# Performance work log

Measured on AMD Instinct MI355X. Metric: run time of the kernel, lower is better.

## Reference

```python
import jax, jax.numpy as jnp
import numpy as np

# Dimensions (match init_kwargs / input_specs)
B, L, HID, NH, HD, PROJ, NL = 4, 1024, 512, 8, 64, 2048, 2
LN_EPS = 1e-5


def _layer_norm(x, g, b):
    m = x.mean(-1, keepdims=True)
    v = ((x - m) ** 2).mean(-1, keepdims=True)
    return (x - m) / jnp.sqrt(v + LN_EPS) * g + b


def setup_inputs() -> dict:
    key = jax.random.key(0)
    ks = jax.random.split(key, 8)
    layer_x = jax.random.normal(ks[0], (B, L, HID), jnp.float32)
    # causal attention mask (True = masked), as built by mask_reshape (triu(1))
    causal = jnp.triu(jnp.ones((L, L), bool), 1)
    full_mask = jnp.broadcast_to(causal[None], (B, L, L))
    mask_multiplier = jnp.ones((B, L, 1), jnp.float32)
    s = 0.02
    qkv_w = (jax.random.normal(ks[1], (NL, HID, 3 * NH * HD), jnp.float32) * s)
    qkv_b = jnp.zeros((NL, 3 * NH * HD), jnp.float32)
    o_w = jax.random.normal(ks[2], (NL, NH * HD, HID), jnp.float32) * s
    o_b = jnp.zeros((NL, HID), jnp.float32)
    ln1_g = jnp.ones((NL, HID), jnp.float32)
    ln1_b = jnp.zeros((NL, HID), jnp.float32)
    ff_w1 = jax.random.normal(ks[3], (NL, HID, PROJ), jnp.float32) * s
    ff_b1 = jnp.zeros((NL, PROJ), jnp.float32)
    ff_w2 = jax.random.normal(ks[4], (NL, PROJ, HID), jnp.float32) * s
    ff_b2 = jnp.zeros((NL, HID), jnp.float32)
    ln2_g = jnp.ones((NL, HID), jnp.float32)
    ln2_b = jnp.zeros((NL, HID), jnp.float32)
    bd_w = jax.random.normal(ks[5], (HID, 1), jnp.float32) * s
    bd_b = jnp.zeros((1,), jnp.float32)
    return dict(layer_x=layer_x, full_mask=full_mask, mask_multiplier=mask_multiplier,
                qkv_w=qkv_w, qkv_b=qkv_b, o_w=o_w, o_b=o_b,
                ln1_g=ln1_g, ln1_b=ln1_b, ff_w1=ff_w1, ff_b1=ff_b1,
                ff_w2=ff_w2, ff_b2=ff_b2, ln2_g=ln2_g, ln2_b=ln2_b,
                bd_w=bd_w, bd_b=bd_b)


def reference(layer_x, full_mask, mask_multiplier, qkv_w, qkv_b, o_w, o_b,
              ln1_g, ln1_b, ff_w1, ff_b1, ff_w2, ff_b2, ln2_g, ln2_b,
              bd_w, bd_b):
    scale = 1.0 / np.sqrt(HD)
    out = layer_x
    for i in range(NL):  # n_layers dense Transformer_Block's (pre_lnorm)
        h = _layer_norm(out, ln1_g[i], ln1_b[i])
        qkv = h @ qkv_w[i] + qkv_b[i]
        q, k, v = jnp.split(qkv, 3, axis=-1)
        q = q.reshape(B, L, NH, HD)
        k = k.reshape(B, L, NH, HD)
        v = v.reshape(B, L, NH, HD)
        scores = jnp.einsum('bqhd,bkhd->bhqk', q, k) * scale
        scores = jnp.where(full_mask[:, None], -1e9, scores)
        attn = jax.nn.softmax(scores, axis=-1)
        av = jnp.einsum('bhqk,bkhd->bqhd', attn, v).reshape(B, L, NH * HD)
        out = out + (av @ o_w[i] + o_b[i])
        # Residual_FF (pre_lnorm)
        h2 = _layer_norm(out, ln2_g[i], ln2_b[i])
        out = out + (jax.nn.relu(h2 @ ff_w1[i] + ff_b1[i]) @ ff_w2[i] + ff_b2[i])
    # BoundaryDecision: per-token keep probability -> hard boundary mask
    bd_prob = jax.nn.sigmoid(out @ bd_w + bd_b)          # (B, L, 1)
    new_mask_multiplier = (bd_prob > 0.5).astype(out.dtype)
    # mode == 'full': blend refined output with the layer input
    new_out = out * mask_multiplier + (1.0 - mask_multiplier) * layer_x
    return new_out, new_mask_multiplier
```

## Files before the change

kernel.cpp:

```cpp
#include <hip/hip_runtime.h>
#include <math.h>

#define BB 4
#define LL 1024
#define HID 512
#define NH 8
#define HD 64
#define PROJ 2048
#define NLAYER 2
#define TOK (BB*LL)
#define QKV3 (3*NH*HD)
#define LN_EPS 1e-5f
#define PSTRIDE ((size_t)TOK * HID)

#define WST     3145728
#define OFF_QKV 0
#define OFF_O   786432
#define OFF_FF1 1048576
#define OFF_FF2 2097152

typedef unsigned short u16;
typedef unsigned int u32;
typedef _Float16 f16;
typedef __attribute__((ext_vector_type(8))) _Float16 half8;
typedef __attribute__((ext_vector_type(4))) float f32x4;

#define MFMAH(a,b,c) __builtin_amdgcn_mfma_f32_16x16x32_f16(a, b, c, 0, 0, 0)

__device__ inline u16 f16_rne(float x) {
    union { f16 h; u16 u; } c; c.h = (f16)x; return c.u;
}

__device__ __forceinline__ void gl16(const u16* g, u16* l) {
    __builtin_amdgcn_global_load_lds(
        (const __attribute__((address_space(1))) unsigned int*)(g),
        (__attribute__((address_space(3))) unsigned int*)(l),
        16, 0, 0);
}

__device__ inline int xcd_swz(int orig, int nwg) {
    int q = nwg >> 3, r = nwg & 7;
    int xcd = orig & 7, idx = orig >> 3;
    return (xcd < r) ? (xcd * (q + 1) + idx)
                     : (r * (q + 1) + (xcd - r) * q + idx);
}

__device__ inline float wave_sum(float v) {
#pragma unroll
    for (int m = 32; m; m >>= 1) v += __shfl_xor(v, m, 64);
    return v;
}

template<int FOLD, int CPY>
__global__ __launch_bounds__(256) void ln_kernel(
    float* __restrict__ x, const float* __restrict__ src,
    const float* __restrict__ P,
    const float* __restrict__ g, const float* __restrict__ b,
    u16* __restrict__ y)
{
    __shared__ float red[4];
    int row = blockIdx.x;
    float* xr = x + (size_t)row * HID;
    int t = threadIdx.x;
    int lane = t & 63, wid = t >> 6;
    float v0, v1;
    if (CPY) {
        const float* sr = src + (size_t)row * HID;
        v0 = sr[t]; v1 = sr[t + 256];
        xr[t] = v0; xr[t + 256] = v1;
    } else {
        v0 = xr[t]; v1 = xr[t + 256];
    }
    if (FOLD > 0) {
        size_t off = (size_t)row * HID + t;
#pragma unroll
        for (int z = 0; z < FOLD; ++z) {
            v0 += P[z * PSTRIDE + off];
            v1 += P[z * PSTRIDE + off + 256];
        }
        xr[t] = v0; xr[t + 256] = v1;
    }
    float s = wave_sum(v0 + v1);
    if (lane == 0) red[wid] = s;
    __syncthreads();
    float mean = (red[0] + red[1] + red[2] + red[3]) * (1.0f / HID);
    __syncthreads();
    float d0 = v0 - mean, d1 = v1 - mean;
    s = wave_sum(d0 * d0 + d1 * d1);
    if (lane == 0) red[wid] = s;
    __syncthreads();
    float var = (red[0] + red[1] + red[2] + red[3]) * (1.0f / HID);
    float rstd = rsqrtf(var + LN_EPS);
    size_t o = (size_t)row * HID;
    y[o + t]       = f16_rne(d0 * rstd * g[t] + b[t]);
    y[o + t + 256] = f16_rne(d1 * rstd * g[t + 256] + b[t + 256]);
}

__global__ __launch_bounds__(256) void wprep_all(
    const float* __restrict__ qkv_w, const float* __restrict__ o_w,
    const float* __restrict__ ff_w1, const float* __restrict__ ff_w2,
    u16* __restrict__ wt)
{
    __shared__ float tile[32][33];
    int bid = blockIdx.x;
    int l = bid / 3072, rem = bid % 3072;
    const float* W; u16* T; int K, N, bx, by;
    if (rem < 768) {
        W = qkv_w + (size_t)l * HID * QKV3;
        T = wt + (size_t)l * WST + OFF_QKV;
        K = HID; N = QKV3; bx = rem % 48; by = rem / 48;
    } else if (rem < 1024) {
        int r2 = rem - 768;
        W = o_w + (size_t)l * HID * HID;
        T = wt + (size_t)l * WST + OFF_O;
        K = HID; N = HID; bx = r2 & 15; by = r2 >> 4;
    } else if (rem < 2048) {
        int r3 = rem - 1024;
        W = ff_w1 + (size_t)l * HID * PROJ;
        T = wt + (size_t)l * WST + OFF_FF1;
        K = HID; N = PROJ; bx = r3 & 63; by = r3 >> 6;
    } else {
        int r4 = rem - 2048;
        W = ff_w2 + (size_t)l * PROJ * HID;
        T = wt + (size_t)l * WST + OFF_FF2;
        K = PROJ; N = HID; bx = r4 & 15; by = r4 >> 4;
    }
    int tx = threadIdx.x & 31, ty = threadIdx.x >> 5;
    int k0 = by * 32, n0 = bx * 32;
#pragma unroll
    for (int r = 0; r < 32; r += 8)
        tile[ty + r][tx] = W[(size_t)(k0 + ty + r) * N + n0 + tx];
    __syncthreads();
#pragma unroll
    for (int r = 0; r < 32; r += 8) {
        float v = tile[tx][ty + r];
        T[(size_t)(n0 + ty + r) * K + k0 + tx] = f16_rne(v);
    }
}

template<int MODE, int SK>
__global__ __launch_bounds__(256) void gemm9(
    const u16* __restrict__ A, const u16* __restrict__ B,
    const float* __restrict__ bias, float* __restrict__ Cf,
    u16* __restrict__ Ch, u16* __restrict__ Cq, u16* __restrict__ Ck,
    u16* __restrict__ Cv, int M, int N, int K)
{
    __shared__ u16 sm[2][(128 + 64) * 64];
    int tid = threadIdx.x;
    int w = tid >> 6, lane = tid & 63;
    int hi = lane >> 4, lo16 = lane & 15;
    int wr = w >> 1, wc = w & 1;

    int gx = gridDim.x, nwg = gx * gridDim.y;
    int swz = xcd_swz(blockIdx.y * gx + blockIdx.x, nwg);
    int row0 = (swz / gx) * 128, col0 = (swz % gx) * 64;

    int kchunk = K / SK;
    int kbeg = blockIdx.z * kchunk;
    int nt = kchunk / 64;

    int srow = lane >> 3;
    int gcol = ((lane & 7) ^ srow) * 8;

    f32x4 acc[4][2] = {};

    for (int t0 = 0; t0 < nt; t0 += 2) {
        __syncthreads();
#pragma unroll
        for (int s = 0; s < 2; ++s) {
            int k0 = kbeg + (t0 + s) * 64;
#pragma unroll
            for (int c = 0; c < 4; ++c) {
                int r0 = w * 32 + c * 8;
                gl16(A + (size_t)(row0 + r0 + srow) * K + k0 + gcol,
                     &sm[s][r0 * 64]);
            }
#pragma unroll
            for (int c = 0; c < 2; ++c) {
                int r0 = w * 16 + c * 8;
                gl16(B + (size_t)(col0 + r0 + srow) * K + k0 + gcol,
                     &sm[s][8192 + r0 * 64]);
            }
        }
        __syncthreads();

#pragma unroll
        for (int s = 0; s < 2; ++s) {
            half8 af[4][2], bf[2][2];
#pragma unroll
            for (int m = 0; m < 4; ++m) {
                int row = wr * 64 + m * 16 + lo16;
#pragma unroll
                for (int ks = 0; ks < 2; ++ks)
                    af[m][ks] = *(const half8*)
                        &sm[s][row * 64 + (((ks * 4 + hi) ^ (row & 7)) * 8)];
            }
#pragma unroll
            for (int n = 0; n < 2; ++n) {
                int row = wc * 32 + n * 16 + lo16;
#pragma unroll
                for (int ks = 0; ks < 2; ++ks)
                    bf[n][ks] = *(const half8*)
                        &sm[s][8192 + row * 64 + (((ks * 4 + hi) ^ (row & 7)) * 8)];
            }
#pragma unroll
            for (int m = 0; m < 4; ++m)
#pragma unroll
                for (int n = 0; n < 2; ++n)
#pragma unroll
                    for (int ks = 0; ks < 2; ++ks)
                        acc[m][n] = MFMAH(af[m][ks], bf[n][ks], acc[m][n]);
        }
    }

    size_t zoff = (size_t)blockIdx.z * M * N;
#pragma unroll
    for (int n = 0; n < 2; ++n) {
        int c = col0 + wc * 32 + n * 16 + lo16;
        float bv = (SK == 1 || blockIdx.z == 0) ? bias[c] : 0.0f;
#pragma unroll
        for (int m = 0; m < 4; ++m) {
            int rbase = row0 + wr * 64 + m * 16 + hi * 4;
#pragma unroll
            for (int r = 0; r < 4; ++r) {
                float x = acc[m][n][r] + bv;
                size_t idx = (size_t)(rbase + r) * N + c;
                if (MODE == 0) {
                    Ch[idx] = f16_rne(x);
                } else if (MODE == 1) {
                    Cf[zoff + idx] = x;
                } else if (MODE == 2) {
                    Ch[idx] = f16_rne(fmaxf(x, 0.0f));
                } else if (MODE == 4) {
                    Cf[idx] += x;
                } else {
                    int tok = rbase + r;
                    int bbv = tok >> 10, tloc = tok & 1023;
                    if (c < HID) {
                        Cq[(((size_t)(bbv * NH + (c >> 6)) * LL + tloc) * HD)
                           + (c & 63)] = f16_rne(x * 0.125f);
                    } else if (c < 2 * HID) {
                        int cc = c - HID;
                        Ck[(((size_t)(bbv * NH + (cc >> 6)) * LL + tloc) * HD)
                           + (cc & 63)] = f16_rne(x);
                    } else {
                        int cc = c - 2 * HID;
                        Cv[(((size_t)(bbv * NH + (cc >> 6)) * HD + (cc & 63)) * LL)
                           + tloc] = f16_rne(x);
                    }
                }
            }
        }
    }
}

__global__ __launch_bounds__(256) void attn9(
    const u16* __restrict__ qP, const u16* __restrict__ kP,
    const u16* __restrict__ vT, u16* __restrict__ avh)
{
    __shared__ u16 Ks[2][64 * 64];
    __shared__ u16 Vt[2][64 * 64];
    __shared__ u16 Pl[4][1024];

    int s = xcd_swz(blockIdx.x, gridDim.x);
    int xcd = s >> 6, u = s & 63;
    int bh_l, qt;
    if (u < 32) { bh_l = u >> 4;            qt = u & 15; }
    else        { bh_l = 2 + ((u - 32) >> 4); qt = 15 - (u & 15); }
    int bh = xcd * 4 + bh_l;
    int bb = bh >> 3, h = bh & 7;
    int tid = threadIdx.x;
    int w = tid >> 6, lane = tid & 63, hi = lane >> 4, lo16 = lane & 15;

    const u16* qsrc = qP + ((size_t)bh * LL + qt * 64 + w * 16 + lo16) * HD;
    half8 qf0 = *(const half8*)(qsrc + hi * 8);
    half8 qf1 = *(const half8*)(qsrc + 32 + hi * 8);

    const u16* kbase = kP + (size_t)bh * LL * HD;
    const u16* vbase = vT + (size_t)bh * HD * LL;

    half8 onesf;
#pragma unroll
    for (int j = 0; j < 8; ++j) onesf[j] = (f16)1.0f;

    f32x4 o[4] = {};
    f32x4 lacc = {};

    int srow8 = lane >> 3;
    int pc = lane & 7;

    for (int g0 = 0; g0 <= qt; g0 += 2) {
        __syncthreads();
#pragma unroll
        for (int sb = 0; sb < 2; ++sb)
#pragma unroll
            for (int c = 0; c < 2; ++c) {
                int r = w * 16 + c * 8 + srow8;
                int lc = (pc ^ (r & 7)) * 8;
                gl16(kbase + (size_t)((g0 + sb) * 64 + r) * HD + lc,
                     &Ks[sb][(w * 16 + c * 8) * 64]);
                gl16(vbase + (size_t)r * LL + (g0 + sb) * 64 + lc,
                     &Vt[sb][(w * 16 + c * 8) * 64]);
            }
        __syncthreads();

#pragma unroll
        for (int sb = 0; sb < 2; ++sb) {
            int g = g0 + sb;
            if (g > qt) break;
            bool diag = (g == qt);
#pragma unroll
            for (int n = 0; n < 4; ++n) {
                int kl = n * 16 + lo16;
                if (diag && n > w) {
#pragma unroll
                    for (int r = 0; r < 4; ++r) {
                        int ql = hi * 4 + r;
                        u32 off = ((u32)(ql * 128 + kl * 2)) ^ ((ql & 7) << 4);
                        *(u16*)((char*)Pl[w] + off) = 0;
                    }
                    continue;
                }
                int tl = n * 16 + lo16;
                half8 kf0 = *(const half8*)&Ks[sb][tl * 64 + ((hi ^ (tl & 7)) * 8)];
                half8 kf1 = *(const half8*)&Ks[sb][tl * 64 + (((4 + hi) ^ (tl & 7)) * 8)];
                f32x4 z = {};
                z = MFMAH(qf0, kf0, z);
                z = MFMAH(qf1, kf1, z);
                if (diag && n == w) {
#pragma unroll
                    for (int r = 0; r < 4; ++r)
                        if (lo16 > hi * 4 + r) z[r] = -1e30f;
                }
#pragma unroll
                for (int r = 0; r < 4; ++r) {
                    float p = __expf(z[r] - 4.0f);
                    int ql = hi * 4 + r;
                    u32 off = ((u32)(ql * 128 + kl * 2)) ^ ((ql & 7) << 4);
                    *(u16*)((char*)Pl[w] + off) = f16_rne(p);
                }
            }
            int cmax = diag ? (w >> 1) : 1;
#pragma unroll
            for (int c = 0; c < 2; ++c) {
                if (c > cmax) break;
                u32 off = ((u32)(lo16 * 128 + c * 64 + hi * 16)) ^ ((lo16 & 7) << 4);
                half8 pa = *(const half8*)((char*)Pl[w] + off);
                lacc = MFMAH(pa, onesf, lacc);
#pragma unroll
                for (int n = 0; n < 4; ++n) {
                    int tl = n * 16 + lo16;
                    half8 vb = *(const half8*)
                        &Vt[sb][tl * 64 + (((c * 4 + hi) ^ (tl & 7)) * 8)];
                    o[n] = MFMAH(pa, vb, o[n]);
                }
            }
        }
    }

#pragma unroll
    for (int r = 0; r < 4; ++r) {
        float inv = 1.0f / lacc[r];
        int tokg = bb * LL + qt * 64 + w * 16 + hi * 4 + r;
#pragma unroll
        for (int n = 0; n < 4; ++n) {
            int d = n * 16 + lo16;
            avh[(size_t)tokg * (NH * HD) + h * HD + d] = f16_rne(o[n][r] * inv);
        }
    }
}

template<int FOLD>
__global__ __launch_bounds__(64) void bd_kernel(
    const float* __restrict__ outb, const float* __restrict__ P,
    const float* __restrict__ layer_x, const float* __restrict__ mm,
    const float* __restrict__ bd_w, const float* __restrict__ bd_b,
    float* __restrict__ d_out)
{
    int t = blockIdx.x;
    int lane = threadIdx.x;
    const float* orow = outb + (size_t)t * HID;
    float mmv = mm[t];
    const float* xrow = layer_x + (size_t)t * HID;
    float* yrow = d_out + (size_t)t * HID;
    float dot = 0.0f;
#pragma unroll
    for (int i = 0; i < 8; ++i) {
        int c = lane + 64 * i;
        float v = orow[c];
        if (FOLD > 0) {
            size_t off = (size_t)t * HID + c;
#pragma unroll
            for (int z = 0; z < FOLD; ++z) v += P[z * PSTRIDE + off];
        }
        dot += v * bd_w[c];
        yrow[c] = v * mmv + (1.0f - mmv) * xrow[c];
    }
    dot = wave_sum(dot);
    if (lane == 0) {
        float z = dot + bd_b[0];
        d_out[(size_t)TOK * HID + t] = (z > 0.0f) ? 1.0f : 0.0f;
    }
}

extern "C" void kernel_launch(void* const* d_in, const int* in_sizes, int n_in,
                              void* d_out, int out_size, void* d_ws, size_t ws_size,
                              hipStream_t stream) {
    const float* layer_x = (const float*)d_in[0];
    const float* mm      = (const float*)d_in[2];
    const float* qkv_w   = (const float*)d_in[3];
    const float* qkv_b   = (const float*)d_in[4];
    const float* o_w     = (const float*)d_in[5];
    const float* o_b     = (const float*)d_in[6];
    const float* ln1_g   = (const float*)d_in[7];
    const float* ln1_b   = (const float*)d_in[8];
    const float* ff_w1   = (const float*)d_in[9];
    const float* ff_b1   = (const float*)d_in[10];
    const float* ff_w2   = (const float*)d_in[11];
    const float* ff_b2   = (const float*)d_in[12];
    const float* ln2_g   = (const float*)d_in[13];
    const float* ln2_b   = (const float*)d_in[14];
    const float* bd_w    = (const float*)d_in[15];
    const float* bd_b    = (const float*)d_in[16];

    char* base = (char*)d_ws;
    float* buf_out = (float*)base;
    u16* hbuf = (u16*)(base + 8388608);
    u16* av   = (u16*)(base + 12582912);
    u16* big  = (u16*)(base + 16777216);
    u16* wt   = (u16*)(base + 33554432);
    float* part = (float*)(base + 46137344);
    u16* vTb  = (u16*)(base + 79691776);
    size_t need = 83886080;
    if (ws_size < need) return;
    u16* qPb  = big;
    u16* kPb  = big + 2097152;
    u16* tbuf = big;

    wprep_all<<<6144, 256, 0, stream>>>(qkv_w, o_w, ff_w1, ff_w2, wt);

    for (int l = 0; l < NLAYER; ++l) {
        size_t wb = (size_t)l * WST;
        if (l == 0)
            ln_kernel<0, 1><<<TOK, 256, 0, stream>>>(
                buf_out, layer_x, nullptr, ln1_g, ln1_b, hbuf);
        else
            ln_kernel<2, 0><<<TOK, 256, 0, stream>>>(
                buf_out, nullptr, part, ln1_g + (size_t)l * HID,
                ln1_b + (size_t)l * HID, hbuf);
        gemm9<3, 1><<<dim3(QKV3 / 64, TOK / 128, 1), 256, 0, stream>>>(
            hbuf, wt + wb + OFF_QKV, qkv_b + (size_t)l * QKV3,
            nullptr, nullptr, qPb, kPb, vTb, TOK, QKV3, HID);
        attn9<<<BB * NH * (LL / 64), 256, 0, stream>>>(qPb, kPb, vTb, av);
        gemm9<4, 1><<<dim3(HID / 64, TOK / 128, 1), 256, 0, stream>>>(
            av, wt + wb + OFF_O, o_b + (size_t)l * HID,
            buf_out, nullptr, nullptr, nullptr, nullptr, TOK, HID, NH * HD);
        ln_kernel<0, 0><<<TOK, 256, 0, stream>>>(
            buf_out, nullptr, nullptr, ln2_g + (size_t)l * HID,
            ln2_b + (size_t)l * HID, hbuf);
        gemm9<2, 1><<<dim3(PROJ / 64, TOK / 128, 1), 256, 0, stream>>>(
            hbuf, wt + wb + OFF_FF1, ff_b1 + (size_t)l * PROJ,
            nullptr, tbuf, nullptr, nullptr, nullptr, TOK, PROJ, HID);
        gemm9<1, 2><<<dim3(HID / 64, TOK / 128, 2), 256, 0, stream>>>(
            tbuf, wt + wb + OFF_FF2, ff_b2 + (size_t)l * HID,
            part, nullptr, nullptr, nullptr, nullptr, TOK, HID, PROJ);
    }

    bd_kernel<2><<<TOK, 64, 0, stream>>>(buf_out, part, layer_x, mm,
                                         bd_w, bd_b, (float*)d_out);
}
```

Before: 212.4 us.

## Accumulate split-K FF2 halves into residual in place instead of partial buffers

```diff
diff --git a/kernel.cpp b/kernel.cpp
--- a/kernel.cpp
+++ b/kernel.cpp
@@ -11,7 +11,6 @@
 #define TOK (BB*LL)
 #define QKV3 (3*NH*HD)
 #define LN_EPS 1e-5f
-#define PSTRIDE ((size_t)TOK * HID)
 
 #define WST     3145728
 #define OFF_QKV 0
@@ -51,10 +50,9 @@
     return v;
 }
 
-template<int FOLD, int CPY>
+template<int CPY>
 __global__ __launch_bounds__(256) void ln_kernel(
     float* __restrict__ x, const float* __restrict__ src,
-    const float* __restrict__ P,
     const float* __restrict__ g, const float* __restrict__ b,
     u16* __restrict__ y)
 {
@@ -66,19 +64,12 @@
     float v0, v1;
     if (CPY) {
         const float* sr = src + (size_t)row * HID;
-        v0 = sr[t]; v1 = sr[t + 256];
-        xr[t] = v0; xr[t + 256] = v1;
+        float2 v = *(const float2*)&sr[2 * t];
+        v0 = v.x; v1 = v.y;
+        *(float2*)&xr[2 * t] = v;
     } else {
-        v0 = xr[t]; v1 = xr[t + 256];
-    }
-    if (FOLD > 0) {
-        size_t off = (size_t)row * HID + t;
-#pragma unroll
-        for (int z = 0; z < FOLD; ++z) {
-            v0 += P[z * PSTRIDE + off];
-            v1 += P[z * PSTRIDE + off + 256];
-        }
-        xr[t] = v0; xr[t + 256] = v1;
+        float2 v = *(const float2*)&xr[2 * t];
+        v0 = v.x; v1 = v.y;
     }
     float s = wave_sum(v0 + v1);
     if (lane == 0) red[wid] = s;
@@ -91,9 +82,11 @@
     __syncthreads();
     float var = (red[0] + red[1] + red[2] + red[3]) * (1.0f / HID);
     float rstd = rsqrtf(var + LN_EPS);
-    size_t o = (size_t)row * HID;
-    y[o + t]       = f16_rne(d0 * rstd * g[t] + b[t]);
-    y[o + t + 256] = f16_rne(d1 * rstd * g[t + 256] + b[t + 256]);
+    float2 gv = *(const float2*)&g[2 * t];
+    float2 bv = *(const float2*)&b[2 * t];
+    u32 pack = (u32)f16_rne(d0 * rstd * gv.x + bv.x)
+             | ((u32)f16_rne(d1 * rstd * gv.y + bv.y) << 16);
+    *(u32*)&y[(size_t)row * HID + 2 * t] = pack;
 }
 
 __global__ __launch_bounds__(256) void wprep_all(
@@ -143,7 +136,7 @@
     const u16* __restrict__ A, const u16* __restrict__ B,
     const float* __restrict__ bias, float* __restrict__ Cf,
     u16* __restrict__ Ch, u16* __restrict__ Cq, u16* __restrict__ Ck,
-    u16* __restrict__ Cv, int M, int N, int K)
+    u16* __restrict__ Cv, int M, int N, int K, int zbase)
 {
     __shared__ u16 sm[2][(128 + 64) * 64];
     int tid = threadIdx.x;
@@ -155,8 +148,9 @@
     int swz = xcd_swz(blockIdx.y * gx + blockIdx.x, nwg);
     int row0 = (swz / gx) * 128, col0 = (swz % gx) * 64;
 
+    int zz = blockIdx.z + zbase;
     int kchunk = K / SK;
-    int kbeg = blockIdx.z * kchunk;
+    int kbeg = zz * kchunk;
     int nt = kchunk / 64;
 
     int srow = lane >> 3;
@@ -213,11 +207,10 @@
         }
     }
 
-    size_t zoff = (size_t)blockIdx.z * M * N;
 #pragma unroll
     for (int n = 0; n < 2; ++n) {
         int c = col0 + wc * 32 + n * 16 + lo16;
-        float bv = (SK == 1 || blockIdx.z == 0) ? bias[c] : 0.0f;
+        float bv = (SK == 1 || zz == 0) ? bias[c] : 0.0f;
 #pragma unroll
         for (int m = 0; m < 4; ++m) {
             int rbase = row0 + wr * 64 + m * 16 + hi * 4;
@@ -227,8 +220,6 @@
                 size_t idx = (size_t)(rbase + r) * N + c;
                 if (MODE == 0) {
                     Ch[idx] = f16_rne(x);
-                } else if (MODE == 1) {
-                    Cf[zoff + idx] = x;
                 } else if (MODE == 2) {
                     Ch[idx] = f16_rne(fmaxf(x, 0.0f));
                 } else if (MODE == 4) {
@@ -370,12 +361,10 @@
     }
 }
 
-template<int FOLD>
 __global__ __launch_bounds__(64) void bd_kernel(
-    const float* __restrict__ outb, const float* __restrict__ P,
-    const float* __restrict__ layer_x, const float* __restrict__ mm,
-    const float* __restrict__ bd_w, const float* __restrict__ bd_b,
-    float* __restrict__ d_out)
+    const float* __restrict__ outb, const float* __restrict__ layer_x,
+    const float* __restrict__ mm, const float* __restrict__ bd_w,
+    const float* __restrict__ bd_b, float* __restrict__ d_out)
 {
     int t = blockIdx.x;
     int lane = threadIdx.x;
@@ -388,11 +377,6 @@
     for (int i = 0; i < 8; ++i) {
         int c = lane + 64 * i;
         float v = orow[c];
-        if (FOLD > 0) {
-            size_t off = (size_t)t * HID + c;
-#pragma unroll
-            for (int z = 0; z < FOLD; ++z) v += P[z * PSTRIDE + off];
-        }
         dot += v * bd_w[c];
         yrow[c] = v * mmv + (1.0f - mmv) * xrow[c];
     }
@@ -429,9 +413,8 @@
     u16* av   = (u16*)(base + 12582912);
     u16* big  = (u16*)(base + 16777216);
     u16* wt   = (u16*)(base + 33554432);
-    float* part = (float*)(base + 46137344);
-    u16* vTb  = (u16*)(base + 79691776);
-    size_t need = 83886080;
+    u16* vTb  = (u16*)(base + 46137344);
+    size_t need = 50331648;
     if (ws_size < need) return;
     u16* qPb  = big;
     u16* kPb  = big + 2097152;
@@ -442,30 +425,33 @@
     for (int l = 0; l < NLAYER; ++l) {
         size_t wb = (size_t)l * WST;
         if (l == 0)
-            ln_kernel<0, 1><<<TOK, 256, 0, stream>>>(
-                buf_out, layer_x, nullptr, ln1_g, ln1_b, hbuf);
+            ln_kernel<1><<<TOK, 256, 0, stream>>>(
+                buf_out, layer_x, ln1_g, ln1_b, hbuf);
         else
-            ln_kernel<2, 0><<<TOK, 256, 0, stream>>>(
-                buf_out, nullptr, part, ln1_g + (size_t)l * HID,
+            ln_kernel<0><<<TOK, 256, 0, stream>>>(
+                buf_out, nullptr, ln1_g + (size_t)l * HID,
                 ln1_b + (size_t)l * HID, hbuf);
         gemm9<3, 1><<<dim3(QKV3 / 64, TOK / 128, 1), 256, 0, stream>>>(
             hbuf, wt + wb + OFF_QKV, qkv_b + (size_t)l * QKV3,
-            nullptr, nullptr, qPb, kPb, vTb, TOK, QKV3, HID);
+            nullptr, nullptr, qPb, kPb, vTb, TOK, QKV3, HID, 0);
         attn9<<<BB * NH * (LL / 64), 256, 0, stream>>>(qPb, kPb, vTb, av);
         gemm9<4, 1><<<dim3(HID / 64, TOK / 128, 1), 256, 0, stream>>>(
             av, wt + wb + OFF_O, o_b + (size_t)l * HID,
-            buf_out, nullptr, nullptr, nullptr, nullptr, TOK, HID, NH * HD);
-        ln_kernel<0, 0><<<TOK, 256, 0, stream>>>(
-            buf_out, nullptr, nullptr, ln2_g + (size_t)l * HID,
+            buf_out, nullptr, nullptr, nullptr, nullptr, TOK, HID, NH * HD, 0);
+        ln_kernel<0><<<TOK, 256, 0, stream>>>(
+            buf_out, nullptr, ln2_g + (size_t)l * HID,
             ln2_b + (size_t)l * HID, hbuf);
         gemm9<2, 1><<<dim3(PROJ / 64, TOK / 128, 1), 256, 0, stream>>>(
             hbuf, wt + wb + OFF_FF1, ff_b1 + (size_t)l * PROJ,
-            nullptr, tbuf, nullptr, nullptr, nullptr, TOK, PROJ, HID);
-        gemm9<1, 2><<<dim3(HID / 64, TOK / 128, 2), 256, 0, stream>>>(
+            nullptr, tbuf, nullptr, nullptr, nullptr, TOK, PROJ, HID, 0);
+        gemm9<4, 2><<<dim3(HID / 64, TOK / 128, 1), 256, 0, stream>>>(
             tbuf, wt + wb + OFF_FF2, ff_b2 + (size_t)l * HID,
-            part, nullptr, nullptr, nullptr, nullptr, TOK, HID, PROJ);
-    }
-
-    bd_kernel<2><<<TOK, 64, 0, stream>>>(buf_out, part, layer_x, mm,
-                                         bd_w, bd_b, (float*)d_out);
-}
+            buf_out, nullptr, nullptr, nullptr, nullptr, TOK, HID, PROJ, 0);
+        gemm9<4, 2><<<dim3(HID / 64, TOK / 128, 1), 256, 0, stream>>>(
+            tbuf, wt + wb + OFF_FF2, ff_b2 + (size_t)l * HID,
+            buf_out, nullptr, nullptr, nullptr, nullptr, TOK, HID, PROJ, 1);
+    }
+
+    bd_kernel<<<TOK, 64, 0, stream>>>(buf_out, layer_x, mm, bd_w, bd_b,
+                                      (float*)d_out);
+}
```

Result: slower. 250.7 us (+18.0%).
